# Performance work log

Hardware: AMD Instinct MI355X
Metric: run time of the kernel (lower is better)

The kernel has to match this reference:

```python
import jax, jax.numpy as jnp
import numpy as np

N_HEAD = 16
HEAD_DIM = 64
NEG_INF = -1e10


def setup_inputs() -> dict:
    key = jax.random.key(0)
    k1, k2, k3 = jax.random.split(key, 3)
    B, S, D = 1, 4096, 1024
    x = jax.random.normal(k1, (B, S, D), dtype=jnp.float32)
    Wqkv = jax.random.normal(k2, (D, 3 * D), dtype=jnp.float32) * 0.02
    bqkv = jnp.zeros((3 * D,), dtype=jnp.float32)
    Wproj = jax.random.normal(k3, (D, D), dtype=jnp.float32) * 0.02
    bproj = jnp.zeros((D,), dtype=jnp.float32)
    return {"x": x, "Wqkv": Wqkv, "bqkv": bqkv, "Wproj": Wproj, "bproj": bproj}


def reference(x, Wqkv, bqkv, Wproj, bproj):
    B, S, D = x.shape
    qkv = x @ Wqkv + bqkv                      # [B, S, 3D]
    q, k, v = jnp.split(qkv, 3, axis=2)
    # split heads -> [B, H, S, Dh]
    def split_heads(t):
        return t.reshape(B, S, N_HEAD, HEAD_DIM).transpose(0, 2, 1, 3)
    q, k, v = split_heads(q), split_heads(k), split_heads(v)
    scale = 1.0 / jnp.sqrt(jnp.float32(HEAD_DIM))
    scores = jnp.einsum('bhqd,bhkd->bhqk', q, k) * scale  # [B, H, S, S]
    causal = jnp.tril(jnp.ones((S, S), dtype=bool))[None, None]
    scores = jnp.where(causal, scores, NEG_INF)
    attn = jax.nn.softmax(scores, axis=-1)
    out = jnp.einsum('bhqk,bhkd->bhqd', attn, v)          # [B, H, S, Dh]
    out = out.transpose(0, 2, 1, 3).reshape(B, S, D)       # merge heads
    return out @ Wproj + bproj
```

## Files before the change

### kernel.cpp

```cpp
#include <hip/hip_runtime.h>
#include <stdint.h>

typedef unsigned short u16;
typedef __bf16 bf16x8 __attribute__((ext_vector_type(8)));
typedef float f32x4 __attribute__((ext_vector_type(4)));

#define S_LEN 4096
#define D_MODEL 1024
#define NHEAD 16
#define HDIM 64

__device__ __forceinline__ u16 f2bf(float f) {
  unsigned u = __builtin_bit_cast(unsigned, f);
  u += 0x7fffu + ((u >> 16) & 1u);
  return (u16)(u >> 16);
}

__device__ __forceinline__ int swz(int row, int col) {
  return (((col >> 3) ^ (row & 7)) << 3) | (col & 7);
}

__device__ __forceinline__ void gload16(const void* g, void* l) {
  auto gp = reinterpret_cast<__attribute__((address_space(1))) void*>(
      reinterpret_cast<uintptr_t>(g));
  auto lp = reinterpret_cast<__attribute__((address_space(3))) void*>(
      static_cast<unsigned>(reinterpret_cast<uintptr_t>(l)));
  __builtin_amdgcn_global_load_lds(gp, lp, 16, 0, 0);
}

__global__ __launch_bounds__(256) void k_conv(const float* __restrict__ in,
                                              u16* __restrict__ out, int n) {
  int i = (blockIdx.x * 256 + threadIdx.x) * 4;
  if (i >= n) return;
  float4 v = *reinterpret_cast<const float4*>(in + i);
  ushort4 o = make_ushort4(f2bf(v.x), f2bf(v.y), f2bf(v.z), f2bf(v.w));
  *reinterpret_cast<ushort4*>(out + i) = o;
}

__global__ __launch_bounds__(256) void k_transpose_conv(const float* __restrict__ in,
                                                        u16* __restrict__ out,
                                                        int R, int C) {
  __shared__ float tile[32][33];
  int c0 = blockIdx.x * 32, r0 = blockIdx.y * 32;
  int tx = threadIdx.x, ty = threadIdx.y;
#pragma unroll
  for (int j = 0; j < 4; ++j)
    tile[ty + j * 8][tx] = in[(size_t)(r0 + ty + j * 8) * C + c0 + tx];
  __syncthreads();
#pragma unroll
  for (int j = 0; j < 4; ++j)
    out[(size_t)(c0 + ty + j * 8) * R + r0 + tx] = f2bf(tile[tx][ty + j * 8]);
}

template <int MODE>
__global__ __launch_bounds__(256) void k_gemm(
    const u16* __restrict__ A, const u16* __restrict__ Bt,
    const float* __restrict__ bias, float* __restrict__ Cf,
    u16* __restrict__ Qd, u16* __restrict__ Kd, u16* __restrict__ Vtd,
    int M, int N, int K) {
  __shared__ __align__(16) u16 lds[2][2 * 128 * 32];
  const int tid = threadIdx.x;
  const int w = tid >> 6, lane = tid & 63;
  const int m0 = blockIdx.y * 128, n0 = blockIdx.x * 128;
  const u16* Atile = A + (size_t)m0 * K;
  const u16* Btile = Bt + (size_t)n0 * K;
  const int r = tid >> 2, c = (tid & 3) * 8;
  const int wm = (w >> 1) * 64, wn = (w & 1) * 64;

  f32x4 acc[4][4] = {};
  const int NT = K / 32;

  {
    const u16* ga = Atile + (size_t)r * K + c;
    const u16* gb = Btile + (size_t)r * K + c;
    u16* lb = lds[0];
    gload16(ga, lb + w * 512);
    gload16(ga + (size_t)64 * K, lb + 2048 + w * 512);
    gload16(gb, lb + 4096 + w * 512);
    gload16(gb + (size_t)64 * K, lb + 4096 + 2048 + w * 512);
  }
  int cur = 0;
  for (int t = 0; t < NT; ++t) {
    __syncthreads();
    if (t + 1 < NT) {
      const u16* ga = Atile + (size_t)r * K + (t + 1) * 32 + c;
      const u16* gb = Btile + (size_t)r * K + (t + 1) * 32 + c;
      u16* lb = lds[cur ^ 1];
      gload16(ga, lb + w * 512);
      gload16(ga + (size_t)64 * K, lb + 2048 + w * 512);
      gload16(gb, lb + 4096 + w * 512);
      gload16(gb + (size_t)64 * K, lb + 4096 + 2048 + w * 512);
    }
    const u16* lA = lds[cur];
    const u16* lB = lds[cur] + 4096;
    bf16x8 af[4], bfv[4];
#pragma unroll
    for (int mi = 0; mi < 4; ++mi)
      af[mi] = *reinterpret_cast<const bf16x8*>(
          lA + (wm + mi * 16 + (lane & 15)) * 32 + (lane >> 4) * 8);
#pragma unroll
    for (int ni = 0; ni < 4; ++ni)
      bfv[ni] = *reinterpret_cast<const bf16x8*>(
          lB + (wn + ni * 16 + (lane & 15)) * 32 + (lane >> 4) * 8);
#pragma unroll
    for (int mi = 0; mi < 4; ++mi)
#pragma unroll
      for (int ni = 0; ni < 4; ++ni)
        acc[mi][ni] = __builtin_amdgcn_mfma_f32_16x16x32_bf16(af[mi], bfv[ni],
                                                              acc[mi][ni], 0, 0, 0);
    cur ^= 1;
  }
#pragma unroll
  for (int mi = 0; mi < 4; ++mi) {
#pragma unroll
    for (int ni = 0; ni < 4; ++ni) {
      int colg = n0 + wn + ni * 16 + (lane & 15);
      float bv = bias[colg];
#pragma unroll
      for (int rr = 0; rr < 4; ++rr) {
        int rowg = m0 + wm + mi * 16 + ((lane >> 4) << 2) + rr;
        float v = acc[mi][ni][rr] + bv;
        if (MODE == 1) {
          Cf[(size_t)rowg * N + colg] = v;
        } else {
          u16 b = f2bf(v);
          if (colg < D_MODEL) {
            int hh = colg >> 6, dd = colg & 63;
            Qd[((size_t)hh * S_LEN + rowg) * 64 + swz(rowg, dd)] = b;
          } else if (colg < 2 * D_MODEL) {
            int cc = colg - D_MODEL;
            int hh = cc >> 6, dd = cc & 63;
            Kd[((size_t)hh * S_LEN + rowg) * 64 + swz(rowg, dd)] = b;
          } else {
            int cc = colg - 2 * D_MODEL;
            int hh = cc >> 6, dd = cc & 63;
            int sl = rowg & 63;
            Vtd[((size_t)hh * 64 + dd) * S_LEN + (rowg & ~63) + swz(dd, sl)] = b;
          }
        }
      }
    }
  }
}

__global__ __launch_bounds__(256) void k_flash(const u16* __restrict__ Qd,
                                               const u16* __restrict__ Kd,
                                               const u16* __restrict__ Vtd,
                                               u16* __restrict__ Ao) {
  __shared__ __align__(16) u16 Ks[2][64 * 64];
  __shared__ __align__(16) u16 Vs[2][64 * 64];
  __shared__ __align__(16) u16 Ps[4][16 * 64];
  const int tid = threadIdx.x, w = tid >> 6, lane = tid & 63;
  const int bid = blockIdx.x;
  const int qt = 63 - (bid >> 4), h = bid & 15;
  const u16* Qh = Qd + (size_t)h * S_LEN * 64;
  const u16* Kh = Kd + (size_t)h * S_LEN * 64;
  const u16* Vh = Vtd + (size_t)h * 64 * S_LEN;
  const int r8 = tid >> 3, c8 = (tid & 7) * 8;
  const float scl2 = 0.125f * 1.44269504088896340736f;

  {
    const u16* gk = Kh + (size_t)r8 * 64 + c8;
    gload16(gk, Ks[0] + w * 512);
    gload16(gk + 32 * 64, Ks[0] + 2048 + w * 512);
    const u16* gv = Vh + (size_t)r8 * S_LEN + c8;
    gload16(gv, Vs[0] + w * 512);
    gload16(gv + (size_t)32 * S_LEN, Vs[0] + 2048 + w * 512);
  }

  bf16x8 qa[2];
  {
    const int rq = qt * 64 + w * 16 + (lane & 15);
#pragma unroll
    for (int kk = 0; kk < 2; ++kk)
      qa[kk] = *reinterpret_cast<const bf16x8*>(
          Qh + (size_t)rq * 64 + swz(rq, kk * 32 + (lane >> 4) * 8));
  }

  float m_run[4], l_run[4];
  f32x4 oacc[4] = {};
#pragma unroll
  for (int rr = 0; rr < 4; ++rr) {
    m_run[rr] = -1e30f;
    l_run[rr] = 0.f;
  }

  __syncthreads();

  int cur = 0;
  for (int j = 0; j <= qt; ++j) {
    if (j < qt) {
      const u16* gk = Kh + ((size_t)((j + 1) * 64 + r8)) * 64 + c8;
      gload16(gk, Ks[cur ^ 1] + w * 512);
      gload16(gk + 32 * 64, Ks[cur ^ 1] + 2048 + w * 512);
      const u16* gv = Vh + (size_t)r8 * S_LEN + (j + 1) * 64 + c8;
      gload16(gv, Vs[cur ^ 1] + w * 512);
      gload16(gv + (size_t)32 * S_LEN, Vs[cur ^ 1] + 2048 + w * 512);
    }

    f32x4 sacc[4] = {};
#pragma unroll
    for (int kk = 0; kk < 2; ++kk) {
#pragma unroll
      for (int ni = 0; ni < 4; ++ni) {
        const int kvl = ni * 16 + (lane & 15);
        bf16x8 kb = *reinterpret_cast<const bf16x8*>(
            Ks[cur] + kvl * 64 + swz(kvl, kk * 32 + (lane >> 4) * 8));
        sacc[ni] = __builtin_amdgcn_mfma_f32_16x16x32_bf16(qa[kk], kb, sacc[ni], 0, 0, 0);
      }
    }

    float pvv[4][4];
#pragma unroll
    for (int ni = 0; ni < 4; ++ni)
#pragma unroll
      for (int rr = 0; rr < 4; ++rr) pvv[ni][rr] = sacc[ni][rr] * scl2;

    if (j == qt) {
      const int rowb = qt * 64 + w * 16 + ((lane >> 4) << 2);
#pragma unroll
      for (int ni = 0; ni < 4; ++ni) {
        const int col = j * 64 + ni * 16 + (lane & 15);
#pragma unroll
        for (int rr = 0; rr < 4; ++rr)
          if (col > rowb + rr) pvv[ni][rr] = -1e30f;
      }
    }

#pragma unroll
    for (int rr = 0; rr < 4; ++rr) {
      float mx = fmaxf(fmaxf(pvv[0][rr], pvv[1][rr]), fmaxf(pvv[2][rr], pvv[3][rr]));
#pragma unroll
      for (int d = 1; d < 16; d <<= 1) mx = fmaxf(mx, __shfl_xor(mx, d));
      float mn = fmaxf(m_run[rr], mx);
      float alpha = exp2f(m_run[rr] - mn);
      m_run[rr] = mn;
      float rs = 0.f;
#pragma unroll
      for (int ni = 0; ni < 4; ++ni) {
        float p = exp2f(pvv[ni][rr] - mn);
        pvv[ni][rr] = p;
        rs += p;
      }
#pragma unroll
      for (int d = 1; d < 16; d <<= 1) rs += __shfl_xor(rs, d);
      l_run[rr] = l_run[rr] * alpha + rs;
#pragma unroll
      for (int ni = 0; ni < 4; ++ni) oacc[ni][rr] *= alpha;
    }

#pragma unroll
    for (int ni = 0; ni < 4; ++ni)
#pragma unroll
      for (int rr = 0; rr < 4; ++rr) {
        int rowl = ((lane >> 4) << 2) + rr;
        int coll = ni * 16 + (lane & 15);
        Ps[w][rowl * 64 + swz(rowl, coll)] = f2bf(pvv[ni][rr]);
      }

#pragma unroll
    for (int kk = 0; kk < 2; ++kk) {
      const int pr = lane & 15;
      bf16x8 pa = *reinterpret_cast<const bf16x8*>(
          Ps[w] + pr * 64 + swz(pr, kk * 32 + (lane >> 4) * 8));
#pragma unroll
      for (int ni = 0; ni < 4; ++ni) {
        const int dd = ni * 16 + (lane & 15);
        bf16x8 vb = *reinterpret_cast<const bf16x8*>(
            Vs[cur] + dd * 64 + swz(dd, kk * 32 + (lane >> 4) * 8));
        oacc[ni] = __builtin_amdgcn_mfma_f32_16x16x32_bf16(pa, vb, oacc[ni], 0, 0, 0);
      }
    }

    __syncthreads();
    cur ^= 1;
  }

#pragma unroll
  for (int rr = 0; rr < 4; ++rr) {
    float inv = 1.f / l_run[rr];
    int rowg = qt * 64 + w * 16 + ((lane >> 4) << 2) + rr;
#pragma unroll
    for (int ni = 0; ni < 4; ++ni) {
      int colg = h * 64 + ni * 16 + (lane & 15);
      Ao[(size_t)rowg * D_MODEL + colg] = f2bf(oacc[ni][rr] * inv);
    }
  }
}

extern "C" void kernel_launch(void* const* d_in, const int* in_sizes, int n_in,
                              void* d_out, int out_size, void* d_ws, size_t ws_size,
                              hipStream_t stream) {
  const float* x = (const float*)d_in[0];
  const float* Wqkv = (const float*)d_in[1];
  const float* bqkv = (const float*)d_in[2];
  const float* Wproj = (const float*)d_in[3];
  const float* bproj = (const float*)d_in[4];
  float* out = (float*)d_out;
  char* ws = (char*)d_ws;

  u16* xb = (u16*)(ws);
  u16* aout = (u16*)(ws);
  u16* wqkvt = (u16*)(ws + (size_t)(8 << 20));
  u16* wprojt = (u16*)(ws + (size_t)(14 << 20));
  u16* Qd = (u16*)(ws + (size_t)(16 << 20));
  u16* Kd = (u16*)(ws + (size_t)(24 << 20));
  u16* Vtd = (u16*)(ws + (size_t)(32 << 20));

  if (ws_size < (size_t)(40 << 20)) return;

  k_conv<<<dim3(4096), dim3(256), 0, stream>>>(x, xb, S_LEN * D_MODEL);
  k_transpose_conv<<<dim3(96, 32), dim3(32, 8), 0, stream>>>(Wqkv, wqkvt, D_MODEL,
                                                             3 * D_MODEL);
  k_transpose_conv<<<dim3(32, 32), dim3(32, 8), 0, stream>>>(Wproj, wprojt, D_MODEL,
                                                             D_MODEL);
  k_gemm<0><<<dim3(24, 32), dim3(256), 0, stream>>>(xb, wqkvt, bqkv, nullptr, Qd, Kd,
                                                    Vtd, S_LEN, 3 * D_MODEL, D_MODEL);
  k_flash<<<dim3(1024), dim3(256), 0, stream>>>(Qd, Kd, Vtd, aout);
  k_gemm<1><<<dim3(8, 32), dim3(256), 0, stream>>>(aout, wprojt, bproj, out, nullptr,
                                                   nullptr, nullptr, S_LEN, D_MODEL,
                                                   D_MODEL);
}
```

Before: 272.0 us.

## Fold softmax scale into Q, defer row-sum reduction, lazily rescale running max

Multiplies Q by scale*log2(e) in the QKV GEMM epilogue, so the flash kernel no longer scales each score. Each lane keeps a partial row sum and does a single shuffle reduction at the end instead of once per KV tile. The running max and the output rescale are updated only when some row's new max exceeds the old one by more than 8 (in log2 units), which skips the alpha exp and accumulator multiply on most tiles. The trade-off is that unnormalized probabilities can reach up to 2^8 before bf16 conversion, which costs some precision, and the wave-wide vote adds a branch.

After: 252.9 us. 7.0% less time.

```diff
diff --git a/kernel.cpp b/kernel.cpp
--- a/kernel.cpp
+++ b/kernel.cpp
@@ -123,15 +123,17 @@
         if (MODE == 1) {
           Cf[(size_t)rowg * N + colg] = v;
         } else {
-          u16 b = f2bf(v);
           if (colg < D_MODEL) {
+            u16 b = f2bf(v * 0.1803368801111f);
             int hh = colg >> 6, dd = colg & 63;
             Qd[((size_t)hh * S_LEN + rowg) * 64 + swz(rowg, dd)] = b;
           } else if (colg < 2 * D_MODEL) {
+            u16 b = f2bf(v);
             int cc = colg - D_MODEL;
             int hh = cc >> 6, dd = cc & 63;
             Kd[((size_t)hh * S_LEN + rowg) * 64 + swz(rowg, dd)] = b;
           } else {
+            u16 b = f2bf(v);
             int cc = colg - 2 * D_MODEL;
             int hh = cc >> 6, dd = cc & 63;
             int sl = rowg & 63;
@@ -157,7 +159,6 @@
   const u16* Kh = Kd + (size_t)h * S_LEN * 64;
   const u16* Vh = Vtd + (size_t)h * 64 * S_LEN;
   const int r8 = tid >> 3, c8 = (tid & 7) * 8;
-  const float scl2 = 0.125f * 1.44269504088896340736f;
 
   {
     const u16* gk = Kh + (size_t)r8 * 64 + c8;
@@ -177,12 +178,12 @@
           Qh + (size_t)rq * 64 + swz(rq, kk * 32 + (lane >> 4) * 8));
   }
 
-  float m_run[4], l_run[4];
+  float m_run[4], l_part[4];
   f32x4 oacc[4] = {};
 #pragma unroll
   for (int rr = 0; rr < 4; ++rr) {
     m_run[rr] = -1e30f;
-    l_run[rr] = 0.f;
+    l_part[rr] = 0.f;
   }
 
   __syncthreads();
@@ -214,7 +215,7 @@
 #pragma unroll
     for (int ni = 0; ni < 4; ++ni)
 #pragma unroll
-      for (int rr = 0; rr < 4; ++rr) pvv[ni][rr] = sacc[ni][rr] * scl2;
+      for (int rr = 0; rr < 4; ++rr) pvv[ni][rr] = sacc[ni][rr];
 
     if (j == qt) {
       const int rowb = qt * 64 + w * 16 + ((lane >> 4) << 2);
@@ -227,26 +228,39 @@
       }
     }
 
+    float mx[4];
 #pragma unroll
     for (int rr = 0; rr < 4; ++rr) {
-      float mx = fmaxf(fmaxf(pvv[0][rr], pvv[1][rr]), fmaxf(pvv[2][rr], pvv[3][rr]));
-#pragma unroll
-      for (int d = 1; d < 16; d <<= 1) mx = fmaxf(mx, __shfl_xor(mx, d));
-      float mn = fmaxf(m_run[rr], mx);
-      float alpha = exp2f(m_run[rr] - mn);
-      m_run[rr] = mn;
+      float m_ = fmaxf(fmaxf(pvv[0][rr], pvv[1][rr]), fmaxf(pvv[2][rr], pvv[3][rr]));
+#pragma unroll
+      for (int d = 1; d < 16; d <<= 1) m_ = fmaxf(m_, __shfl_xor(m_, d));
+      mx[rr] = m_;
+    }
+
+    bool need = (mx[0] > m_run[0] + 8.f) | (mx[1] > m_run[1] + 8.f) |
+                (mx[2] > m_run[2] + 8.f) | (mx[3] > m_run[3] + 8.f);
+    if (__any(need)) {
+#pragma unroll
+      for (int rr = 0; rr < 4; ++rr) {
+        float mn = fmaxf(m_run[rr], mx[rr]);
+        float alpha = exp2f(m_run[rr] - mn);
+        m_run[rr] = mn;
+        l_part[rr] *= alpha;
+#pragma unroll
+        for (int ni = 0; ni < 4; ++ni) oacc[ni][rr] *= alpha;
+      }
+    }
+
+#pragma unroll
+    for (int rr = 0; rr < 4; ++rr) {
       float rs = 0.f;
 #pragma unroll
       for (int ni = 0; ni < 4; ++ni) {
-        float p = exp2f(pvv[ni][rr] - mn);
+        float p = exp2f(pvv[ni][rr] - m_run[rr]);
         pvv[ni][rr] = p;
         rs += p;
       }
-#pragma unroll
-      for (int d = 1; d < 16; d <<= 1) rs += __shfl_xor(rs, d);
-      l_run[rr] = l_run[rr] * alpha + rs;
-#pragma unroll
-      for (int ni = 0; ni < 4; ++ni) oacc[ni][rr] *= alpha;
+      l_part[rr] += rs;
     }
 
 #pragma unroll
@@ -278,7 +292,10 @@
 
 #pragma unroll
   for (int rr = 0; rr < 4; ++rr) {
-    float inv = 1.f / l_run[rr];
+    float l = l_part[rr];
+#pragma unroll
+    for (int d = 1; d < 16; d <<= 1) l += __shfl_xor(l, d);
+    float inv = 1.f / l;
     int rowg = qt * 64 + w * 16 + ((lane >> 4) << 2) + rr;
 #pragma unroll
     for (int ni = 0; ni < 4; ++ni) {
```

## Compute transposed scores to keep P in registers, skip LDS round-trip

Applied to the files above, without the earlier changes.

The QK^T MFMA operands are swapped so each lane holds a column of scores for one query. The exponentiated probabilities can then be packed with v_cvt_pk_bf16 straight into the A operand of the PV MFMA, with no shared-memory staging. To make this work, V^T is stored with a permuted key order (sigma64), and the softmax scale times log2(e) is folded into Q at projection time. A lazy rescale updates the running max and oacc only when the max grows by more than 8 (in log2 units), and the row-sum reduction is deferred to the end. This removes per-tile LDS writes, reads and shuffles. The costs are that p values can grow up to 2^8 before rescaling and the code depends on the new layout conventions.

Result: faster. 226.9 us (-16.6%).

```diff
diff --git a/kernel.cpp b/kernel.cpp
--- a/kernel.cpp
+++ b/kernel.cpp
@@ -2,8 +2,10 @@
 #include <stdint.h>
 
 typedef unsigned short u16;
+typedef unsigned u32;
 typedef __bf16 bf16x8 __attribute__((ext_vector_type(8)));
 typedef float f32x4 __attribute__((ext_vector_type(4)));
+typedef u32 u32x4 __attribute__((ext_vector_type(4)));
 
 #define S_LEN 4096
 #define D_MODEL 1024
@@ -16,8 +18,19 @@
   return (u16)(u >> 16);
 }
 
+__device__ __forceinline__ u32 cvt_pk_bf16(float lo, float hi) {
+  u32 r;
+  asm("v_cvt_pk_bf16_f32 %0, %1, %2" : "=v"(r) : "v"(lo), "v"(hi));
+  return r;
+}
+
 __device__ __forceinline__ int swz(int row, int col) {
   return (((col >> 3) ^ (row & 7)) << 3) | (col & 7);
+}
+
+__device__ __forceinline__ int sigma64(int s) {
+  int a = s >> 4;
+  return ((a >> 1) << 5) | (((s >> 2) & 3) << 3) | ((a & 1) << 2) | (s & 3);
 }
 
 __device__ __forceinline__ void gload16(const void* g, void* l) {
@@ -123,19 +136,21 @@
         if (MODE == 1) {
           Cf[(size_t)rowg * N + colg] = v;
         } else {
-          u16 b = f2bf(v);
           if (colg < D_MODEL) {
+            u16 b = f2bf(v * 0.1803368801111f);
             int hh = colg >> 6, dd = colg & 63;
             Qd[((size_t)hh * S_LEN + rowg) * 64 + swz(rowg, dd)] = b;
           } else if (colg < 2 * D_MODEL) {
+            u16 b = f2bf(v);
             int cc = colg - D_MODEL;
             int hh = cc >> 6, dd = cc & 63;
             Kd[((size_t)hh * S_LEN + rowg) * 64 + swz(rowg, dd)] = b;
           } else {
+            u16 b = f2bf(v);
             int cc = colg - 2 * D_MODEL;
             int hh = cc >> 6, dd = cc & 63;
-            int sl = rowg & 63;
-            Vtd[((size_t)hh * 64 + dd) * S_LEN + (rowg & ~63) + swz(dd, sl)] = b;
+            int csl = sigma64(rowg & 63);
+            Vtd[((size_t)hh * 64 + dd) * S_LEN + (rowg & ~63) + swz(dd, csl)] = b;
           }
         }
       }
@@ -149,7 +164,6 @@
                                                u16* __restrict__ Ao) {
   __shared__ __align__(16) u16 Ks[2][64 * 64];
   __shared__ __align__(16) u16 Vs[2][64 * 64];
-  __shared__ __align__(16) u16 Ps[4][16 * 64];
   const int tid = threadIdx.x, w = tid >> 6, lane = tid & 63;
   const int bid = blockIdx.x;
   const int qt = 63 - (bid >> 4), h = bid & 15;
@@ -157,7 +171,7 @@
   const u16* Kh = Kd + (size_t)h * S_LEN * 64;
   const u16* Vh = Vtd + (size_t)h * 64 * S_LEN;
   const int r8 = tid >> 3, c8 = (tid & 7) * 8;
-  const float scl2 = 0.125f * 1.44269504088896340736f;
+  const int g = lane >> 4, ql = lane & 15;
 
   {
     const u16* gk = Kh + (size_t)r8 * 64 + c8;
@@ -170,20 +184,15 @@
 
   bf16x8 qa[2];
   {
-    const int rq = qt * 64 + w * 16 + (lane & 15);
+    const int rq = qt * 64 + w * 16 + ql;
 #pragma unroll
     for (int kk = 0; kk < 2; ++kk)
       qa[kk] = *reinterpret_cast<const bf16x8*>(
-          Qh + (size_t)rq * 64 + swz(rq, kk * 32 + (lane >> 4) * 8));
-  }
-
-  float m_run[4], l_run[4];
+          Qh + (size_t)rq * 64 + swz(rq, kk * 32 + g * 8));
+  }
+
+  float m_run = -1e30f, l_part = 0.f;
   f32x4 oacc[4] = {};
-#pragma unroll
-  for (int rr = 0; rr < 4; ++rr) {
-    m_run[rr] = -1e30f;
-    l_run[rr] = 0.f;
-  }
 
   __syncthreads();
 
@@ -203,10 +212,10 @@
     for (int kk = 0; kk < 2; ++kk) {
 #pragma unroll
       for (int ni = 0; ni < 4; ++ni) {
-        const int kvl = ni * 16 + (lane & 15);
+        const int kvl = ni * 16 + ql;
         bf16x8 kb = *reinterpret_cast<const bf16x8*>(
-            Ks[cur] + kvl * 64 + swz(kvl, kk * 32 + (lane >> 4) * 8));
-        sacc[ni] = __builtin_amdgcn_mfma_f32_16x16x32_bf16(qa[kk], kb, sacc[ni], 0, 0, 0);
+            Ks[cur] + kvl * 64 + swz(kvl, kk * 32 + g * 8));
+        sacc[ni] = __builtin_amdgcn_mfma_f32_16x16x32_bf16(kb, qa[kk], sacc[ni], 0, 0, 0);
       }
     }
 
@@ -214,60 +223,67 @@
 #pragma unroll
     for (int ni = 0; ni < 4; ++ni)
 #pragma unroll
-      for (int rr = 0; rr < 4; ++rr) pvv[ni][rr] = sacc[ni][rr] * scl2;
+      for (int rr = 0; rr < 4; ++rr) pvv[ni][rr] = sacc[ni][rr];
 
     if (j == qt) {
-      const int rowb = qt * 64 + w * 16 + ((lane >> 4) << 2);
+      const int qoff = w * 16 + ql;
+#pragma unroll
+      for (int ni = 0; ni < 4; ++ni)
+#pragma unroll
+        for (int rr = 0; rr < 4; ++rr)
+          if (ni * 16 + g * 4 + rr > qoff) pvv[ni][rr] = -1e30f;
+    }
+
+    float mx;
+    {
+      float a0 = fmaxf(fmaxf(pvv[0][0], pvv[0][1]), fmaxf(pvv[0][2], pvv[0][3]));
+      float a1 = fmaxf(fmaxf(pvv[1][0], pvv[1][1]), fmaxf(pvv[1][2], pvv[1][3]));
+      float a2 = fmaxf(fmaxf(pvv[2][0], pvv[2][1]), fmaxf(pvv[2][2], pvv[2][3]));
+      float a3 = fmaxf(fmaxf(pvv[3][0], pvv[3][1]), fmaxf(pvv[3][2], pvv[3][3]));
+      mx = fmaxf(fmaxf(a0, a1), fmaxf(a2, a3));
+      mx = fmaxf(mx, __shfl_xor(mx, 16));
+      mx = fmaxf(mx, __shfl_xor(mx, 32));
+    }
+
+    if (__any(mx > m_run + 8.f)) {
+      float mn = fmaxf(m_run, mx);
+      float alpha = exp2f(m_run - mn);
+      m_run = mn;
+      l_part *= alpha;
+      float ao[4];
+#pragma unroll
+      for (int rr = 0; rr < 4; ++rr) ao[rr] = __shfl(alpha, g * 4 + rr);
+#pragma unroll
+      for (int ni = 0; ni < 4; ++ni)
+#pragma unroll
+        for (int rr = 0; rr < 4; ++rr) oacc[ni][rr] *= ao[rr];
+    }
+
+    u32 pk[4][2];
+    {
+      float rs = 0.f;
 #pragma unroll
       for (int ni = 0; ni < 4; ++ni) {
-        const int col = j * 64 + ni * 16 + (lane & 15);
-#pragma unroll
-        for (int rr = 0; rr < 4; ++rr)
-          if (col > rowb + rr) pvv[ni][rr] = -1e30f;
-      }
-    }
-
-#pragma unroll
-    for (int rr = 0; rr < 4; ++rr) {
-      float mx = fmaxf(fmaxf(pvv[0][rr], pvv[1][rr]), fmaxf(pvv[2][rr], pvv[3][rr]));
-#pragma unroll
-      for (int d = 1; d < 16; d <<= 1) mx = fmaxf(mx, __shfl_xor(mx, d));
-      float mn = fmaxf(m_run[rr], mx);
-      float alpha = exp2f(m_run[rr] - mn);
-      m_run[rr] = mn;
-      float rs = 0.f;
+        float p0 = exp2f(pvv[ni][0] - m_run);
+        float p1 = exp2f(pvv[ni][1] - m_run);
+        float p2 = exp2f(pvv[ni][2] - m_run);
+        float p3 = exp2f(pvv[ni][3] - m_run);
+        rs += (p0 + p1) + (p2 + p3);
+        pk[ni][0] = cvt_pk_bf16(p0, p1);
+        pk[ni][1] = cvt_pk_bf16(p2, p3);
+      }
+      l_part += rs;
+    }
+
+#pragma unroll
+    for (int kk2 = 0; kk2 < 2; ++kk2) {
+      u32x4 pw = {pk[2 * kk2][0], pk[2 * kk2][1], pk[2 * kk2 + 1][0], pk[2 * kk2 + 1][1]};
+      bf16x8 pa = __builtin_bit_cast(bf16x8, pw);
 #pragma unroll
       for (int ni = 0; ni < 4; ++ni) {
-        float p = exp2f(pvv[ni][rr] - mn);
-        pvv[ni][rr] = p;
-        rs += p;
-      }
-#pragma unroll
-      for (int d = 1; d < 16; d <<= 1) rs += __shfl_xor(rs, d);
-      l_run[rr] = l_run[rr] * alpha + rs;
-#pragma unroll
-      for (int ni = 0; ni < 4; ++ni) oacc[ni][rr] *= alpha;
-    }
-
-#pragma unroll
-    for (int ni = 0; ni < 4; ++ni)
-#pragma unroll
-      for (int rr = 0; rr < 4; ++rr) {
-        int rowl = ((lane >> 4) << 2) + rr;
-        int coll = ni * 16 + (lane & 15);
-        Ps[w][rowl * 64 + swz(rowl, coll)] = f2bf(pvv[ni][rr]);
-      }
-
-#pragma unroll
-    for (int kk = 0; kk < 2; ++kk) {
-      const int pr = lane & 15;
-      bf16x8 pa = *reinterpret_cast<const bf16x8*>(
-          Ps[w] + pr * 64 + swz(pr, kk * 32 + (lane >> 4) * 8));
-#pragma unroll
-      for (int ni = 0; ni < 4; ++ni) {
-        const int dd = ni * 16 + (lane & 15);
+        const int dd = ni * 16 + ql;
         bf16x8 vb = *reinterpret_cast<const bf16x8*>(
-            Vs[cur] + dd * 64 + swz(dd, kk * 32 + (lane >> 4) * 8));
+            Vs[cur] + dd * 64 + swz(dd, kk2 * 32 + g * 8));
         oacc[ni] = __builtin_amdgcn_mfma_f32_16x16x32_bf16(pa, vb, oacc[ni], 0, 0, 0);
       }
     }
@@ -276,14 +292,22 @@
     cur ^= 1;
   }
 
-#pragma unroll
-  for (int rr = 0; rr < 4; ++rr) {
-    float inv = 1.f / l_run[rr];
-    int rowg = qt * 64 + w * 16 + ((lane >> 4) << 2) + rr;
-#pragma unroll
-    for (int ni = 0; ni < 4; ++ni) {
-      int colg = h * 64 + ni * 16 + (lane & 15);
-      Ao[(size_t)rowg * D_MODEL + colg] = f2bf(oacc[ni][rr] * inv);
+  {
+    float l = l_part;
+    l += __shfl_xor(l, 16);
+    l += __shfl_xor(l, 32);
+    float inv = 1.f / l;
+    float io[4];
+#pragma unroll
+    for (int rr = 0; rr < 4; ++rr) io[rr] = __shfl(inv, g * 4 + rr);
+#pragma unroll
+    for (int rr = 0; rr < 4; ++rr) {
+      int rowg = qt * 64 + w * 16 + g * 4 + rr;
+#pragma unroll
+      for (int ni = 0; ni < 4; ++ni) {
+        int colg = h * 64 + ni * 16 + ql;
+        Ao[(size_t)rowg * D_MODEL + colg] = f2bf(oacc[ni][rr] * io[rr]);
+      }
     }
   }
 }
```
